# Optimization experiments

Measured on AMD Instinct MI355X. Metric: run time of the kernel, lower is better.

Reference implementation:

```python
import jax, jax.numpy as jnp
import numpy as np
from jax import lax

B, C, H, W = 64, 512, 14, 14
HEAD_DIM = 32
NUM_HEADS = C // HEAD_DIM
HIDDEN = int(C * 4.0)
EPS = 1e-5
LS_INIT = 1e-5


def setup_inputs() -> dict:
    key = jax.random.key(0)
    ks = jax.random.split(key, 16)
    d = {}
    d['x'] = jax.random.normal(ks[0], (B, C, H, W), dtype=jnp.float32)
    # shared BatchNorm2d(dim) (inference-mode, running stats)
    d['bn_g'] = 1.0 + 0.1 * jax.random.normal(ks[1], (C,), dtype=jnp.float32)
    d['bn_b'] = 0.1 * jax.random.normal(ks[2], (C,), dtype=jnp.float32)
    d['bn_m'] = 0.1 * jax.random.normal(ks[3], (C,), dtype=jnp.float32)
    d['bn_v'] = jax.random.uniform(ks[4], (C,), minval=0.5, maxval=1.5, dtype=jnp.float32)
    # MHSA params (qkv_bias=False)
    d['qkv_w'] = 0.02 * jax.random.normal(ks[5], (3 * C, C), dtype=jnp.float32)
    d['proj_w'] = 0.02 * jax.random.normal(ks[6], (C, C), dtype=jnp.float32)
    d['proj_b'] = jnp.zeros((C,), dtype=jnp.float32)
    # ConvFFN: depthwise 7x7 (groups=C, no bias) -> BN -> 1x1 -> GELU -> 1x1
    d['dw_w'] = 0.02 * jax.random.normal(ks[7], (C, 1, 7, 7), dtype=jnp.float32)
    d['fbn_g'] = 1.0 + 0.1 * jax.random.normal(ks[8], (C,), dtype=jnp.float32)
    d['fbn_b'] = 0.1 * jax.random.normal(ks[9], (C,), dtype=jnp.float32)
    d['fbn_m'] = 0.1 * jax.random.normal(ks[10], (C,), dtype=jnp.float32)
    d['fbn_v'] = jax.random.uniform(ks[11], (C,), minval=0.5, maxval=1.5, dtype=jnp.float32)
    d['fc1_w'] = 0.02 * jax.random.normal(ks[12], (HIDDEN, C), dtype=jnp.float32)
    d['fc1_b'] = jnp.zeros((HIDDEN,), dtype=jnp.float32)
    d['fc2_w'] = 0.02 * jax.random.normal(ks[13], (C, HIDDEN), dtype=jnp.float32)
    d['fc2_b'] = jnp.zeros((C,), dtype=jnp.float32)
    # layer scale params, shape (C,1,1)
    d['ls1'] = LS_INIT * jnp.ones((C, 1, 1), dtype=jnp.float32)
    d['ls2'] = LS_INIT * jnp.ones((C, 1, 1), dtype=jnp.float32)
    return d


def _bn2d(x, g, b, m, v):
    # inference BatchNorm2d over channel dim of NCHW
    inv = g * lax.rsqrt(v + EPS)
    return x * inv[None, :, None, None] + (b - m * inv)[None, :, None, None]


def _mhsa(x, qkv_w, proj_w, proj_b):
    b, c, h, w = x.shape
    n = h * w
    xt = x.reshape(b, c, n).transpose(0, 2, 1)              # [B,N,C]
    qkv = xt @ qkv_w.T                                       # [B,N,3C]
    qkv = qkv.reshape(b, n, 3, NUM_HEADS, HEAD_DIM).transpose(2, 0, 3, 1, 4)
    q, k, v = qkv[0], qkv[1], qkv[2]                         # [B,h,N,d]
    scale = HEAD_DIM ** -0.5
    attn = jax.nn.softmax(jnp.einsum('bhnd,bhmd->bhnm', q * scale, k), axis=-1)
    o = jnp.einsum('bhnm,bhmd->bhnd', attn, v)               # [B,h,N,d]
    o = o.transpose(0, 2, 1, 3).reshape(b, n, c)             # [B,N,C]
    o = o @ proj_w.T + proj_b
    return o.transpose(0, 2, 1).reshape(b, c, h, w)


def _convffn(x, dw_w, fbn_g, fbn_b, fbn_m, fbn_v, fc1_w, fc1_b, fc2_w, fc2_b):
    y = lax.conv_general_dilated(x, dw_w, window_strides=(1, 1),
                                 padding=[(3, 3), (3, 3)],
                                 feature_group_count=C,
                                 dimension_numbers=('NCHW', 'OIHW', 'NCHW'))
    y = _bn2d(y, fbn_g, fbn_b, fbn_m, fbn_v)
    y = jnp.einsum('bchw,oc->bohw', y, fc1_w) + fc1_b[None, :, None, None]
    y = jax.nn.gelu(y, approximate=False)
    y = jnp.einsum('bchw,oc->bohw', y, fc2_w) + fc2_b[None, :, None, None]
    return y


def reference(x, bn_g, bn_b, bn_m, bn_v, qkv_w, proj_w, proj_b,
              dw_w, fbn_g, fbn_b, fbn_m, fbn_v, fc1_w, fc1_b, fc2_w, fc2_b,
              ls1, ls2):
    xn = _bn2d(x, bn_g, bn_b, bn_m, bn_v)
    x = x + ls1[None] * _mhsa(xn, qkv_w, proj_w, proj_b)
    xn = _bn2d(x, bn_g, bn_b, bn_m, bn_v)
    x = x + ls2[None] * _convffn(xn, dw_w, fbn_g, fbn_b, fbn_m, fbn_v,
                                 fc1_w, fc1_b, fc2_w, fc2_b)
    return x
```

## Files before the change

kernel.cpp:

```cpp
#include <hip/hip_runtime.h>
#include <hip/hip_bf16.h>
#include <hip/hip_fp8.h>
#include <stdint.h>

#define NTOK 196
#define NB   64
#define CCH  512
#define HID  2048
#define MTOT (NB * NTOK)

typedef __attribute__((ext_vector_type(8))) short  short8v;
typedef __attribute__((ext_vector_type(4))) float  float4v;
typedef __attribute__((ext_vector_type(2))) int    int2v;


__device__ __forceinline__ void mfma_fp8(float4v& d, int2v a, int2v b) {
  asm("v_mfma_f32_16x16x32_fp8_fp8 %0, %1, %2, %0" : "+v"(d) : "v"(a), "v"(b));
}

__device__ __forceinline__ void gload_lds16(const void* gsrc, void* ldst) {
  __builtin_amdgcn_global_load_lds(
      (const __attribute__((address_space(1))) unsigned int*)gsrc,
      (__attribute__((address_space(3))) unsigned int*)ldst, 16, 0, 0);
}

__device__ __forceinline__ int swz4(int r) { return (r ^ (r >> 2)) & 3; }

__device__ __forceinline__ uint32_t cvt2_fp8(float a, float b) {
  uint32_t d;
  asm("v_cvt_pk_fp8_f32 %0, %1, %2" : "=v"(d) : "v"(a), "v"(b));
  return d;
}

__device__ __forceinline__ uint8_t to_fp8(float v) {
  return __hip_fp8_e4m3(v).__x;
}


__global__ void prep_consts(const float* __restrict__ bn_g, const float* __restrict__ bn_b,
                            const float* __restrict__ bn_m, const float* __restrict__ bn_v,
                            const float* __restrict__ fbn_g, const float* __restrict__ fbn_b,
                            const float* __restrict__ fbn_m, const float* __restrict__ fbn_v,
                            float* __restrict__ cst) {
  int c = blockIdx.x * blockDim.x + threadIdx.x;
  if (c < CCH) {
    float i1 = bn_g[c] * rsqrtf(bn_v[c] + 1e-5f);
    cst[c] = i1;
    cst[512 + c] = bn_b[c] - bn_m[c] * i1;
    float i2 = fbn_g[c] * rsqrtf(fbn_v[c] + 1e-5f);
    cst[1024 + c] = i2;
    cst[1536 + c] = fbn_b[c] - fbn_m[c] * i2;
  }
}


__global__ void cvt_weights(const float* __restrict__ qkv_w, const float* __restrict__ proj_w,
                            const float* __restrict__ fc1_w, const float* __restrict__ fc2_w,
                            uint8_t* __restrict__ qkvb, uint8_t* __restrict__ projb,
                            uint8_t* __restrict__ fc1b, uint8_t* __restrict__ fc2b) {
  int i4 = blockIdx.x * blockDim.x + threadIdx.x;
  const int nq = 1536 * 512 / 4;
  const int np = 512 * 512 / 4;
  const int n1 = 2048 * 512 / 4;
  const float* src;
  uint8_t* dst;
  int k;
  if (i4 < nq)                { src = qkv_w;  dst = qkvb;  k = i4; }
  else if (i4 < nq + np)      { src = proj_w; dst = projb; k = i4 - nq; }
  else if (i4 < nq + np + n1) { src = fc1_w;  dst = fc1b;  k = i4 - nq - np; }
  else                        { src = fc2_w;  dst = fc2b;  k = i4 - nq - np - n1; }
  float4v v = *(const float4v*)(src + 4 * (size_t)k);
  uint32_t w0 = cvt2_fp8(v[0] * 16.0f, v[1] * 16.0f);
  uint32_t w1 = cvt2_fp8(v[2] * 16.0f, v[3] * 16.0f);
  *(uint16_t*)(dst + 4 * (size_t)k)     = (uint16_t)w0;
  *(uint16_t*)(dst + 4 * (size_t)k + 2) = (uint16_t)w1;
}


__global__ __launch_bounds__(256) void transpose_x(
    const float* __restrict__ x, uint8_t* __restrict__ xnt8,
    __hip_bfloat16* __restrict__ xt, const float* __restrict__ cst) {
  __shared__ float tile[32][33];
  const int n0 = blockIdx.x * 32;
  const int c0 = blockIdx.y * 32;
  const int b  = blockIdx.z;
  const int j = threadIdx.x & 31, i = threadIdx.x >> 5;
  #pragma unroll
  for (int p = 0; p < 4; ++p) {
    int cc = c0 + i + p * 8;
    int n = n0 + j;
    if (n < NTOK) tile[i + p * 8][j] = x[((size_t)b * CCH + cc) * NTOK + n];
  }
  __syncthreads();
  const float s = cst[c0 + j], t = cst[512 + c0 + j];
  float bn[4];
  size_t off[4];
  bool ok[4];
  #pragma unroll
  for (int p = 0; p < 4; ++p) {
    int n = n0 + i + p * 8;
    int cc = c0 + j;
    ok[p] = (n < NTOK);
    if (ok[p]) {
      float raw = tile[j][i + p * 8];
      size_t o = ((size_t)b * NTOK + n) * CCH + cc;
      xt[o] = __float2bfloat16(raw);
      bn[p] = raw * s + t;
      off[p] = o;
    }
  }
  uint32_t w0 = cvt2_fp8(bn[0], bn[1]);
  uint32_t w1 = cvt2_fp8(bn[2], bn[3]);
  if (ok[0]) xnt8[off[0]] = (uint8_t)w0;
  if (ok[1]) xnt8[off[1]] = (uint8_t)(w0 >> 8);
  if (ok[2]) xnt8[off[2]] = (uint8_t)w1;
  if (ok[3]) xnt8[off[3]] = (uint8_t)(w1 >> 8);
}


template<int EPI>
__global__ __launch_bounds__(256, 3) void gemm8f(
    const uint8_t* __restrict__ A, const uint8_t* __restrict__ Bw,
    int N, int K, int NY,
    __hip_bfloat16* __restrict__ outb, uint8_t* __restrict__ out8,
    float* __restrict__ outf,
    const float* __restrict__ bias, const float* __restrict__ ls,
    const __hip_bfloat16* __restrict__ resid) {
  __shared__ char lds[49152];
  const int tid  = threadIdx.x;
  const int lane = tid & 63;
  const int wave = tid >> 6;

  const int q    = (int)gridDim.x >> 3;
  const int orig = blockIdx.x;
  const int wgid = (orig & 7) * q + (orig >> 3);
  const int bx = wgid / NY;
  const int by = wgid - bx * NY;

  const int m0 = bx * 128;
  const int n0 = by * 128;
  const int wm = (wave >> 1) * 64;
  const int wn = (wave & 1) * 64;
  const int KT = K >> 6;

  float4v acc[4][4] = {};

  auto stage = [&](int buf, int kt) {
    const int kb = kt * 64;
    char* base = lds + buf * 16384;
    #pragma unroll
    for (int i = 0; i < 2; ++i) {
      int L = i * 4096 + tid * 16;
      int row = L >> 6;
      int lc = ((L >> 4) & 3) ^ swz4(row);
      gload_lds16(A + (size_t)(m0 + row) * K + kb + lc * 16, base + L);
    }
    #pragma unroll
    for (int i = 0; i < 2; ++i) {
      int L = i * 4096 + tid * 16;
      int row = L >> 6;
      int lc = ((L >> 4) & 3) ^ swz4(row);
      gload_lds16(Bw + (size_t)(n0 + row) * K + kb + lc * 16, base + 8192 + L);
    }
  };

  auto compute = [&](int buf) {
    const char* bA = lds + buf * 16384;
    const char* bB = bA + 8192;
    const int g = lane >> 4;
    #pragma unroll
    for (int t = 0; t < 2; ++t) {
      int2v av[4], bv[4];
      #pragma unroll
      for (int f = 0; f < 4; ++f) {
        int row = wm + f * 16 + (lane & 15);
        int c16 = ((t << 1) | (g >> 1)) ^ swz4(row);
        av[f] = *(const int2v*)(bA + row * 64 + c16 * 16 + (g & 1) * 8);
      }
      #pragma unroll
      for (int j = 0; j < 4; ++j) {
        int row = wn + j * 16 + (lane & 15);
        int c16 = ((t << 1) | (g >> 1)) ^ swz4(row);
        bv[j] = *(const int2v*)(bB + row * 64 + c16 * 16 + (g & 1) * 8);
      }
      #pragma unroll
      for (int i = 0; i < 4; ++i)
        #pragma unroll
        for (int j = 0; j < 4; ++j)
          mfma_fp8(acc[i][j], av[i], bv[j]);
    }
  };

  stage(0, 0);
  stage(1, 1);
  int cur = 0;
  for (int kt = 0; kt < KT - 1; ++kt) {
    asm volatile("s_waitcnt vmcnt(4)" ::: "memory");
    __builtin_amdgcn_s_barrier();
    __builtin_amdgcn_sched_barrier(0);
    if (kt + 2 < KT) {
      int s = cur + 2; if (s >= 3) s -= 3;
      stage(s, kt + 2);
    }
    compute(cur);
    ++cur; if (cur == 3) cur = 0;
  }
  asm volatile("s_waitcnt vmcnt(0)" ::: "memory");
  __builtin_amdgcn_s_barrier();
  __builtin_amdgcn_sched_barrier(0);
  compute(cur);
  asm volatile("s_nop 7\n\ts_nop 7");

  const float RS = 0.0625f;

  if (EPI == 0) {
    #pragma unroll
    for (int i = 0; i < 4; ++i)
      #pragma unroll
      for (int j = 0; j < 4; ++j)
        #pragma unroll
        for (int r = 0; r < 4; r += 2) {
          int m = m0 + wm + i * 16 + ((lane >> 4) << 2) + r;
          int n = n0 + wn + j * 16 + (lane & 15);
          int bb = m / NTOK, tok = m - bb * NTOK;
          int bb2 = (m + 1) / NTOK, tok2 = (m + 1) - bb2 * NTOK;
          int sel = n >> 9, hh = (n >> 5) & 15, d = n & 31;
          uint32_t w = cvt2_fp8(acc[i][j][r] * RS, acc[i][j][r + 1] * RS);
          out8[(((size_t)(sel * 16 + hh) * NB + bb) * NTOK + tok) * 32 + d]  = (uint8_t)w;
          out8[(((size_t)(sel * 16 + hh) * NB + bb2) * NTOK + tok2) * 32 + d] = (uint8_t)(w >> 8);
        }
  } else if (EPI == 2) {
    #pragma unroll
    for (int i = 0; i < 4; ++i)
      #pragma unroll
      for (int j = 0; j < 4; ++j)
        #pragma unroll
        for (int r = 0; r < 4; r += 2) {
          int m = m0 + wm + i * 16 + ((lane >> 4) << 2) + r;
          int n = n0 + wn + j * 16 + (lane & 15);
          float z0 = acc[i][j][r] * RS + bias[n];
          float z1 = acc[i][j][r + 1] * RS + bias[n];
          float g0 = z0 / (1.0f + __expf(-1.702f * z0));
          float g1 = z1 / (1.0f + __expf(-1.702f * z1));
          uint32_t w = cvt2_fp8(g0, g1);
          out8[(size_t)m * N + n]       = (uint8_t)w;
          out8[(size_t)(m + 1) * N + n] = (uint8_t)(w >> 8);
        }
  } else if (EPI == 1) {
    #pragma unroll
    for (int i = 0; i < 4; ++i)
      #pragma unroll
      for (int j = 0; j < 4; ++j)
        #pragma unroll
        for (int r = 0; r < 4; ++r) {
          int m = m0 + wm + i * 16 + ((lane >> 4) << 2) + r;
          int n = n0 + wn + j * 16 + (lane & 15);
          float v = acc[i][j][r] * RS + bias[n];
          v = __bfloat162float(resid[(size_t)m * CCH + n]) + ls[n] * v;
          outb[(size_t)m * CCH + n] = __float2bfloat16(v);
        }
  } else {
    float* LT = (float*)lds;
    #pragma unroll 1
    for (int hh = 0; hh < 2; ++hh) {
      __syncthreads();
      if ((wn >> 6) == hh) {
        #pragma unroll
        for (int i = 0; i < 4; ++i)
          #pragma unroll
          for (int j = 0; j < 4; ++j)
            #pragma unroll
            for (int r = 0; r < 4; ++r) {
              int ml = wm + i * 16 + ((lane >> 4) << 2) + r;
              int nl = j * 16 + (lane & 15);
              int n = n0 + wn + nl;
              float v = acc[i][j][r] * RS + bias[n];
              v = __bfloat162float(resid[(size_t)(m0 + ml) * CCH + n]) + ls[n] * v;
              LT[nl * 129 + ml] = v;
            }
      }
      __syncthreads();
      {
        int ml0 = lane << 1;
        int mg = m0 + ml0;
        int bb0 = mg / NTOK;
        int tt0 = mg - bb0 * NTOK;
        int bb1 = (mg + 1) / NTOK;
        int tt1 = (mg + 1) - bb1 * NTOK;
        size_t base0 = (size_t)bb0 * (CCH * NTOK) + tt0;
        size_t base1 = (size_t)bb1 * (CCH * NTOK) + tt1;
        #pragma unroll
        for (int u = 0; u < 16; ++u) {
          int cr = wave * 16 + u;
          int cg = n0 + hh * 64 + cr;
          float v0 = LT[cr * 129 + ml0];
          float v1 = LT[cr * 129 + ml0 + 1];
          outf[base0 + (size_t)cg * NTOK] = v0;
          outf[base1 + (size_t)cg * NTOK] = v1;
        }
      }
    }
  }
}


__global__ __launch_bounds__(256, 3) void attn_kernel(
    const uint8_t* __restrict__ qkv8, uint8_t* __restrict__ o_t8) {
  __shared__ char sQ[208 * 48];
  __shared__ char sK[224 * 48];
  __shared__ char sV[32 * 240];
  __shared__ char sP[4][16 * 232];
  const int tid  = threadIdx.x;
  const int lane = tid & 63;
  const int wave = tid >> 6;
  const int b = blockIdx.x >> 4;
  const int h = blockIdx.x & 15;
  const size_t CHB = 6272;
  const uint8_t* Qg = qkv8 + ((size_t)(0 * 16 + h) * NB + b) * CHB;
  const uint8_t* Kg = qkv8 + ((size_t)(1 * 16 + h) * NB + b) * CHB;
  const uint8_t* Vg = qkv8 + ((size_t)(2 * 16 + h) * NB + b) * CHB;

  for (int i = tid; i < 144; i += 256) {
    int r = i / 12, w = i % 12;
    ((uint32_t*)(sQ + (196 + r) * 48))[w] = 0u;
  }
  for (int i = tid; i < 336; i += 256) {
    int r = i / 12, w = i % 12;
    ((uint32_t*)(sK + (196 + r) * 48))[w] = 0u;
  }
  for (int i = tid; i < 352; i += 256) {
    int d = i / 11, w = i % 11;
    ((uint32_t*)(sV + d * 240 + 196))[w] = 0u;
  }

  for (int c = tid; c < 392; c += 256) {
    int row = c >> 1, hf = c & 1;
    uint4 vq = *(const uint4*)(Qg + c * 16);
    *(uint4*)(sQ + row * 48 + hf * 16) = vq;
    uint4 vk = *(const uint4*)(Kg + c * 16);
    *(uint4*)(sK + row * 48 + hf * 16) = vk;
  }
  for (int u = tid; u < 784; u += 256) {
    int row = u >> 2, d0 = (u & 3) * 8;
    uint64_t w = *(const uint64_t*)(Vg + (size_t)u * 8);
    #pragma unroll
    for (int e = 0; e < 8; ++e)
      sV[(d0 + e) * 240 + row] = (char)(w >> (8 * e));
  }
  __syncthreads();

  const float scale = 0.17677669529663687f;
  char* Pw = sP[wave];
  const int g = lane >> 4;

  for (int mt = wave; mt < 13; mt += 4) {
    int qrow = mt * 16 + (lane & 15);
    int2v aq = *(const int2v*)(sQ + qrow * 48 + g * 8);

    float4v s[14];
    #pragma unroll
    for (int nt = 0; nt < 14; ++nt) {
      int krow = nt * 16 + (lane & 15);
      int2v bk = *(const int2v*)(sK + krow * 48 + g * 8);
      s[nt] = float4v{0.f, 0.f, 0.f, 0.f};
      mfma_fp8(s[nt], aq, bk);
    }
    asm volatile("s_nop 7\n\ts_nop 7");

    float mx[4] = {-INFINITY, -INFINITY, -INFINITY, -INFINITY};
    #pragma unroll
    for (int nt = 0; nt < 14; ++nt) {
      bool valid = (nt * 16 + (lane & 15)) < NTOK;
      #pragma unroll
      for (int r = 0; r < 4; ++r) {
        float v = valid ? s[nt][r] * scale : -INFINITY;
        s[nt][r] = v;
        mx[r] = fmaxf(mx[r], v);
      }
    }
    #pragma unroll
    for (int off = 1; off < 16; off <<= 1) {
      #pragma unroll
      for (int r = 0; r < 4; ++r) mx[r] = fmaxf(mx[r], __shfl_xor(mx[r], off));
    }
    float sum[4] = {0.f, 0.f, 0.f, 0.f};
    #pragma unroll
    for (int nt = 0; nt < 14; ++nt) {
      #pragma unroll
      for (int r = 0; r < 4; ++r) {
        float e = __expf(s[nt][r] - mx[r]);
        s[nt][r] = e;
        sum[r] += e;
      }
    }
    #pragma unroll
    for (int off = 1; off < 16; off <<= 1) {
      #pragma unroll
      for (int r = 0; r < 4; ++r) sum[r] += __shfl_xor(sum[r], off);
    }
    float rs[4];
    #pragma unroll
    for (int r = 0; r < 4; ++r) rs[r] = 1.0f / sum[r];

    #pragma unroll
    for (int nt = 0; nt < 14; ++nt) {
      int col = nt * 16 + (lane & 15);
      #pragma unroll
      for (int r = 0; r < 4; r += 2) {
        int prow = ((lane >> 4) << 2) + r;
        uint32_t w = cvt2_fp8(s[nt][r], s[nt][r + 1]);
        *(uint8_t*)(Pw + prow * 232 + col)       = (uint8_t)w;
        *(uint8_t*)(Pw + (prow + 1) * 232 + col) = (uint8_t)(w >> 8);
      }
    }

    float4v o0 = float4v{0.f, 0.f, 0.f, 0.f};
    float4v o1 = float4v{0.f, 0.f, 0.f, 0.f};
    #pragma unroll
    for (int ks = 0; ks < 7; ++ks) {
      int2v pa = *(const int2v*)(Pw + (lane & 15) * 232 + ks * 32 + g * 8);
      int2v v0 = *(const int2v*)(sV + (lane & 15) * 240 + ks * 32 + g * 8);
      int2v v1 = *(const int2v*)(sV + (16 + (lane & 15)) * 240 + ks * 32 + g * 8);
      mfma_fp8(o0, pa, v0);
      mfma_fp8(o1, pa, v1);
    }
    asm volatile("s_nop 7\n\ts_nop 7");

    #pragma unroll
    for (int r = 0; r < 4; ++r) {
      int trow = mt * 16 + ((lane >> 4) << 2) + r;
      if (trow < NTOK) {
        size_t ob = ((size_t)b * NTOK + trow) * CCH + h * 32 + (lane & 15);
        uint32_t w = cvt2_fp8(o0[r] * rs[r], o1[r] * rs[r]);
        o_t8[ob]      = (uint8_t)w;
        o_t8[ob + 16] = (uint8_t)(w >> 8);
      }
    }
  }
}


__global__ __launch_bounds__(448) void dwconv_tm(
    const __hip_bfloat16* __restrict__ x1t, const float* __restrict__ dw_w,
    const float* __restrict__ cst, uint8_t* __restrict__ yt8) {
  __shared__ float img[196][32];
  __shared__ float wgt[49][32];
  const int tid = threadIdx.x;
  const int b  = blockIdx.x >> 4;
  const int cb = (blockIdx.x & 15) * 32;
  const int c  = tid & 31;
  const int gc = cb + c;
  const float s = cst[gc], t0 = cst[512 + gc];
  #pragma unroll
  for (int k = 0; k < 14; ++k) {
    int p = (tid >> 5) + k * 14;
    img[p][c] = __bfloat162float(x1t[((size_t)b * NTOK + p) * CCH + gc]) * s + t0;
  }
  for (int i = tid; i < 49 * 32; i += 448) {
    int tap = i >> 5, cc = i & 31;
    wgt[tap][cc] = dw_w[(cb + cc) * 49 + tap];
  }
  __syncthreads();

  const int px = tid >> 5;
  float out[14];
  #pragma unroll
  for (int i = 0; i < 14; ++i) out[i] = 0.f;
  #pragma unroll 1
  for (int row = 0; row < 14; ++row) {
    float v[7];
    #pragma unroll
    for (int dx = 0; dx < 7; ++dx) {
      int ix = px + dx - 3;
      v[dx] = ((unsigned)ix < 14u) ? img[row * 14 + ix][c] : 0.f;
    }
    #pragma unroll
    for (int kk = 0; kk < 7; ++kk) {
      int py = row + 3 - kk;
      if (py >= 0 && py < 14) {
        float hsum = 0.f;
        #pragma unroll
        for (int dx = 0; dx < 7; ++dx) hsum = fmaf(v[dx], wgt[kk * 7 + dx][c], hsum);
        out[py] += hsum;
      }
    }
  }
  const float fs = cst[1024 + gc], ft = cst[1536 + gc];
  #pragma unroll
  for (int py = 0; py < 14; py += 2) {
    uint32_t w = cvt2_fp8(out[py] * fs + ft, out[py + 1] * fs + ft);
    yt8[((size_t)b * NTOK + py * 14 + px) * CCH + gc]       = (uint8_t)w;
    yt8[((size_t)b * NTOK + (py + 1) * 14 + px) * CCH + gc] = (uint8_t)(w >> 8);
  }
}


extern "C" void kernel_launch(void* const* d_in, const int* in_sizes, int n_in,
                              void* d_out, int out_size, void* d_ws, size_t ws_size,
                              hipStream_t stream) {
  const float* x      = (const float*)d_in[0];
  const float* bn_g   = (const float*)d_in[1];
  const float* bn_b   = (const float*)d_in[2];
  const float* bn_m   = (const float*)d_in[3];
  const float* bn_v   = (const float*)d_in[4];
  const float* qkv_w  = (const float*)d_in[5];
  const float* proj_w = (const float*)d_in[6];
  const float* proj_b = (const float*)d_in[7];
  const float* dw_w   = (const float*)d_in[8];
  const float* fbn_g  = (const float*)d_in[9];
  const float* fbn_b  = (const float*)d_in[10];
  const float* fbn_m  = (const float*)d_in[11];
  const float* fbn_v  = (const float*)d_in[12];
  const float* fc1_w  = (const float*)d_in[13];
  const float* fc1_b  = (const float*)d_in[14];
  const float* fc2_w  = (const float*)d_in[15];
  const float* fc2_b  = (const float*)d_in[16];
  const float* ls1    = (const float*)d_in[17];
  const float* ls2    = (const float*)d_in[18];

  char* ws = (char*)d_ws;
  float* cst             = (float*)ws;
  uint8_t* qkvb8         = (uint8_t*)(ws + 32768);
  uint8_t* projb8        = (uint8_t*)(ws + 819200);
  uint8_t* fc1b8         = (uint8_t*)(ws + 1081344);
  uint8_t* fc2b8         = (uint8_t*)(ws + 2129920);
  uint8_t* xnt8          = (uint8_t*)(ws + 3178496);
  __hip_bfloat16* xt     = (__hip_bfloat16*)(ws + 9601024);
  uint8_t* qkv8          = (uint8_t*)(ws + 22446080);
  uint8_t* ot8           = (uint8_t*)(ws + 60981248);
  __hip_bfloat16* x1t    = (__hip_bfloat16*)(ws + 67403776);
  uint8_t* yt8           = (uint8_t*)(ws + 80248832);
  uint8_t* h8            = (uint8_t*)(ws + 3178496);

  prep_consts<<<dim3(2), dim3(256), 0, stream>>>(bn_g, bn_b, bn_m, bn_v,
                                                 fbn_g, fbn_b, fbn_m, fbn_v, cst);
  cvt_weights<<<dim3(3072), dim3(256), 0, stream>>>(qkv_w, proj_w, fc1_w, fc2_w,
                                                    qkvb8, projb8, fc1b8, fc2b8);
  transpose_x<<<dim3(7, 16, 64), dim3(256), 0, stream>>>(x, xnt8, xt, cst);
  gemm8f<0><<<dim3(1176), dim3(256), 0, stream>>>(xnt8, qkvb8, 1536, 512, 12,
                                                  nullptr, qkv8, nullptr, nullptr, nullptr, nullptr);
  attn_kernel<<<dim3(1024), dim3(256), 0, stream>>>(qkv8, ot8);
  gemm8f<1><<<dim3(392), dim3(256), 0, stream>>>(ot8, projb8, 512, 512, 4,
                                                 x1t, nullptr, nullptr, proj_b, ls1, xt);
  dwconv_tm<<<dim3(1024), dim3(448), 0, stream>>>(x1t, dw_w, cst, yt8);
  gemm8f<2><<<dim3(1568), dim3(256), 0, stream>>>(yt8, fc1b8, 2048, 512, 16,
                                                  nullptr, h8, nullptr, fc1_b, nullptr, nullptr);
  gemm8f<3><<<dim3(392), dim3(256), 0, stream>>>(h8, fc2b8, 512, 2048, 4,
                                                 nullptr, nullptr, (float*)d_out, fc2_b, ls2, x1t);
}
```

Baseline: 195.2 us.

## Fuse FFN fc1, GELU and fc2 into one kernel keeping hidden activations in LDS

Replaces the separate fc1 (GELU epilogue) and fc2 GEMM launches with a single kernel. Each 512-thread block owns 64 tokens and loops over four 512-wide hidden chunks, keeping each GELU'd fp8 chunk in shared memory and accumulating fc2 in registers. Weight tiles are double-buffered through 128KB of LDS. This removes the global round trip of the 12544x2048 hidden tensor and one launch. In exchange only 196 blocks run at one block per CU, which limits occupancy and latency hiding.

```diff
diff --git a/kernel.cpp b/kernel.cpp
--- a/kernel.cpp
+++ b/kernel.cpp
@@ -30,10 +30,6 @@
   uint32_t d;
   asm("v_cvt_pk_fp8_f32 %0, %1, %2" : "=v"(d) : "v"(a), "v"(b));
   return d;
-}
-
-__device__ __forceinline__ uint8_t to_fp8(float v) {
-  return __hip_fp8_e4m3(v).__x;
 }
 
 
@@ -123,7 +119,6 @@
     const uint8_t* __restrict__ A, const uint8_t* __restrict__ Bw,
     int N, int K, int NY,
     __hip_bfloat16* __restrict__ outb, uint8_t* __restrict__ out8,
-    float* __restrict__ outf,
     const float* __restrict__ bias, const float* __restrict__ ls,
     const __hip_bfloat16* __restrict__ resid) {
   __shared__ char lds[49152];
@@ -229,24 +224,7 @@
           out8[(((size_t)(sel * 16 + hh) * NB + bb) * NTOK + tok) * 32 + d]  = (uint8_t)w;
           out8[(((size_t)(sel * 16 + hh) * NB + bb2) * NTOK + tok2) * 32 + d] = (uint8_t)(w >> 8);
         }
-  } else if (EPI == 2) {
-    #pragma unroll
-    for (int i = 0; i < 4; ++i)
-      #pragma unroll
-      for (int j = 0; j < 4; ++j)
-        #pragma unroll
-        for (int r = 0; r < 4; r += 2) {
-          int m = m0 + wm + i * 16 + ((lane >> 4) << 2) + r;
-          int n = n0 + wn + j * 16 + (lane & 15);
-          float z0 = acc[i][j][r] * RS + bias[n];
-          float z1 = acc[i][j][r + 1] * RS + bias[n];
-          float g0 = z0 / (1.0f + __expf(-1.702f * z0));
-          float g1 = z1 / (1.0f + __expf(-1.702f * z1));
-          uint32_t w = cvt2_fp8(g0, g1);
-          out8[(size_t)m * N + n]       = (uint8_t)w;
-          out8[(size_t)(m + 1) * N + n] = (uint8_t)(w >> 8);
-        }
-  } else if (EPI == 1) {
+  } else {
     #pragma unroll
     for (int i = 0; i < 4; ++i)
       #pragma unroll
@@ -259,46 +237,156 @@
           v = __bfloat162float(resid[(size_t)m * CCH + n]) + ls[n] * v;
           outb[(size_t)m * CCH + n] = __float2bfloat16(v);
         }
-  } else {
-    float* LT = (float*)lds;
+  }
+}
+
+
+__global__ __launch_bounds__(512, 1) void ffn_fused(
+    const uint8_t* __restrict__ yt8, const uint8_t* __restrict__ w1,
+    const uint8_t* __restrict__ w2, const float* __restrict__ b1,
+    const float* __restrict__ b2, const float* __restrict__ ls2,
+    const __hip_bfloat16* __restrict__ resid, float* __restrict__ outf) {
+  __shared__ char lds[131072];
+  char* sA = lds;
+  char* sH = lds + 32768;
+  char* sB = lds + 65536;
+  const int tid  = threadIdx.x;
+  const int lane = tid & 63;
+  const int wv   = tid >> 6;
+  const int g    = lane >> 4;
+  const int l15  = lane & 15;
+  const int m0   = blockIdx.x * 64;
+  const float RS = 0.0625f;
+
+  #pragma unroll
+  for (int u = 0; u < 4; ++u) {
+    int L = u * 8192 + tid * 16;
+    int r = L >> 9;
+    int pc = (L >> 4) & 31;
+    int lc = pc ^ (r & 31);
+    gload_lds16(yt8 + (size_t)(m0 + r) * 512 + lc * 16, sA + L);
+  }
+
+  auto stageB = [&](const uint8_t* W, int rs, int kb, int buf) {
+    char* base = sB + buf * 32768;
+    #pragma unroll
+    for (int u = 0; u < 4; ++u) {
+      int L = u * 8192 + tid * 16;
+      int r = L >> 6;
+      int pc = (L >> 4) & 3;
+      int lc = pc ^ swz4(r);
+      gload_lds16(W + (size_t)r * rs + kb + lc * 16, base + L);
+    }
+  };
+
+  auto step = [&](const char* Asrc, int ks, int buf, float4v (&acc)[4][4]) {
+    const char* bB = sB + buf * 32768;
+    #pragma unroll
+    for (int t = 0; t < 2; ++t) {
+      int2v av[4], bv[4];
+      #pragma unroll
+      for (int f = 0; f < 4; ++f) {
+        int r = f * 16 + l15;
+        int c = ks * 4 + t * 2 + (g >> 1);
+        int pc = c ^ (r & 31);
+        av[f] = *(const int2v*)(Asrc + r * 512 + pc * 16 + (g & 1) * 8);
+      }
+      #pragma unroll
+      for (int j = 0; j < 4; ++j) {
+        int r = wv * 64 + j * 16 + l15;
+        int c16 = ((t << 1) | (g >> 1)) ^ swz4(r);
+        bv[j] = *(const int2v*)(bB + r * 64 + c16 * 16 + (g & 1) * 8);
+      }
+      #pragma unroll
+      for (int f = 0; f < 4; ++f)
+        #pragma unroll
+        for (int j = 0; j < 4; ++j)
+          mfma_fp8(acc[f][j], av[f], bv[j]);
+    }
+  };
+
+  float4v acc2[4][4] = {};
+
+  stageB(w1, 512, 0, 0);
+  __syncthreads();
+  int par = 0;
+
+  #pragma unroll 1
+  for (int nh = 0; nh < 4; ++nh) {
+    const uint8_t* W1c = w1 + (size_t)nh * 512 * 512;
+    float4v acc1[4][4] = {};
     #pragma unroll 1
-    for (int hh = 0; hh < 2; ++hh) {
+    for (int ks = 0; ks < 8; ++ks) {
+      if (ks < 7) stageB(W1c, 512, (ks + 1) * 64, par ^ 1);
+      else        stageB(w2, 2048, nh * 512, par ^ 1);
+      step(sA, ks, par, acc1);
       __syncthreads();
-      if ((wn >> 6) == hh) {
+      par ^= 1;
+    }
+    #pragma unroll
+    for (int i = 0; i < 4; ++i)
+      #pragma unroll
+      for (int j = 0; j < 4; ++j) {
+        int n = wv * 64 + j * 16 + l15;
+        float bias1 = b1[nh * 512 + n];
         #pragma unroll
-        for (int i = 0; i < 4; ++i)
+        for (int r = 0; r < 4; r += 2) {
+          int m = i * 16 + (g << 2) + r;
+          float z0 = acc1[i][j][r] * RS + bias1;
+          float z1 = acc1[i][j][r + 1] * RS + bias1;
+          float g0 = z0 / (1.0f + __expf(-1.702f * z0));
+          float g1 = z1 / (1.0f + __expf(-1.702f * z1));
+          uint32_t w = cvt2_fp8(g0, g1);
+          int pc0 = ((n >> 4) ^ (m & 31)) * 16 + (n & 15);
+          int pc1 = ((n >> 4) ^ ((m + 1) & 31)) * 16 + (n & 15);
+          sH[m * 512 + pc0]       = (uint8_t)w;
+          sH[(m + 1) * 512 + pc1] = (uint8_t)(w >> 8);
+        }
+      }
+    __syncthreads();
+    #pragma unroll 1
+    for (int ks = 0; ks < 8; ++ks) {
+      if (ks < 7)      stageB(w2, 2048, nh * 512 + (ks + 1) * 64, par ^ 1);
+      else if (nh < 3) stageB(w1 + (size_t)(nh + 1) * 512 * 512, 512, 0, par ^ 1);
+      step(sH, ks, par, acc2);
+      __syncthreads();
+      par ^= 1;
+    }
+  }
+  asm volatile("s_nop 7\n\ts_nop 7");
+
+  #pragma unroll 1
+  for (int p = 0; p < 2; ++p) {
+    __syncthreads();
+    if ((wv >> 2) == p) {
+      float* LT = (float*)(lds + (wv & 3) * 17408);
+      #pragma unroll
+      for (int i = 0; i < 4; ++i)
+        #pragma unroll
+        for (int j = 0; j < 4; ++j)
           #pragma unroll
-          for (int j = 0; j < 4; ++j)
-            #pragma unroll
-            for (int r = 0; r < 4; ++r) {
-              int ml = wm + i * 16 + ((lane >> 4) << 2) + r;
-              int nl = j * 16 + (lane & 15);
-              int n = n0 + wn + nl;
-              float v = acc[i][j][r] * RS + bias[n];
-              v = __bfloat162float(resid[(size_t)(m0 + ml) * CCH + n]) + ls[n] * v;
-              LT[nl * 129 + ml] = v;
-            }
-      }
-      __syncthreads();
-      {
-        int ml0 = lane << 1;
-        int mg = m0 + ml0;
-        int bb0 = mg / NTOK;
-        int tt0 = mg - bb0 * NTOK;
-        int bb1 = (mg + 1) / NTOK;
-        int tt1 = (mg + 1) - bb1 * NTOK;
-        size_t base0 = (size_t)bb0 * (CCH * NTOK) + tt0;
-        size_t base1 = (size_t)bb1 * (CCH * NTOK) + tt1;
-        #pragma unroll
-        for (int u = 0; u < 16; ++u) {
-          int cr = wave * 16 + u;
-          int cg = n0 + hh * 64 + cr;
-          float v0 = LT[cr * 129 + ml0];
-          float v1 = LT[cr * 129 + ml0 + 1];
-          outf[base0 + (size_t)cg * NTOK] = v0;
-          outf[base1 + (size_t)cg * NTOK] = v1;
-        }
-      }
+          for (int r = 0; r < 4; ++r) {
+            int ml = i * 16 + (g << 2) + r;
+            int nl = j * 16 + l15;
+            int n2 = wv * 64 + nl;
+            float v = acc2[i][j][r] * RS + b2[n2];
+            v = __bfloat162float(resid[(size_t)(m0 + ml) * CCH + n2]) + ls2[n2] * v;
+            LT[nl * 68 + ml] = v;
+          }
+    }
+    __syncthreads();
+    #pragma unroll
+    for (int u = 0; u < 8; ++u) {
+      int idx = tid + 512 * u;
+      int s = idx >> 10;
+      int nl = (idx >> 4) & 63;
+      int mq = idx & 15;
+      const float* LT = (const float*)(lds + s * 17408);
+      float4v v4 = *(const float4v*)(LT + nl * 68 + mq * 4);
+      int n2 = (p * 4 + s) * 64 + nl;
+      int m = m0 + mq * 4;
+      int bb = m / NTOK, tok = m - bb * NTOK;
+      *(float4v*)(outf + (size_t)bb * (CCH * NTOK) + (size_t)n2 * NTOK + tok) = v4;
     }
   }
 }
@@ -530,7 +618,6 @@
   uint8_t* ot8           = (uint8_t*)(ws + 60981248);
   __hip_bfloat16* x1t    = (__hip_bfloat16*)(ws + 67403776);
   uint8_t* yt8           = (uint8_t*)(ws + 80248832);
-  uint8_t* h8            = (uint8_t*)(ws + 3178496);
 
   prep_consts<<<dim3(2), dim3(256), 0, stream>>>(bn_g, bn_b, bn_m, bn_v,
                                                  fbn_g, fbn_b, fbn_m, fbn_v, cst);
@@ -538,13 +625,11 @@
                                                     qkvb8, projb8, fc1b8, fc2b8);
   transpose_x<<<dim3(7, 16, 64), dim3(256), 0, stream>>>(x, xnt8, xt, cst);
   gemm8f<0><<<dim3(1176), dim3(256), 0, stream>>>(xnt8, qkvb8, 1536, 512, 12,
-                                                  nullptr, qkv8, nullptr, nullptr, nullptr, nullptr);
+                                                  nullptr, qkv8, nullptr, nullptr, nullptr);
   attn_kernel<<<dim3(1024), dim3(256), 0, stream>>>(qkv8, ot8);
   gemm8f<1><<<dim3(392), dim3(256), 0, stream>>>(ot8, projb8, 512, 512, 4,
-                                                 x1t, nullptr, nullptr, proj_b, ls1, xt);
+                                                 x1t, nullptr, proj_b, ls1, xt);
   dwconv_tm<<<dim3(1024), dim3(448), 0, stream>>>(x1t, dw_w, cst, yt8);
-  gemm8f<2><<<dim3(1568), dim3(256), 0, stream>>>(yt8, fc1b8, 2048, 512, 16,
-                                                  nullptr, h8, nullptr, fc1_b, nullptr, nullptr);
-  gemm8f<3><<<dim3(392), dim3(256), 0, stream>>>(h8, fc2b8, 512, 2048, 4,
-                                                 nullptr, nullptr, (float*)d_out, fc2_b, ls2, x1t);
-}
+  ffn_fused<<<dim3(196), dim3(512), 0, stream>>>(yt8, fc1b8, fc2b8, fc1_b, fc2_b,
+                                                 ls2, x1t, (float*)d_out);
+}
```

Result: slower. 209.9 us (+7.6%).
